# Kernel tuning notes

Measured on AMD Instinct MI355X. Metric: run time of the kernel, lower is better.

Reference implementation:

```python
import jax, jax.numpy as jnp
import numpy as np

B, D, U, M, K = 8192, 512, 512, 16, 64


def setup_inputs() -> dict:
    key = jax.random.key(0)
    ks = jax.random.split(key, 5)
    return {
        "x": jax.random.normal(ks[0], (B, D), dtype=jnp.float32),
        "key_kernel": jax.random.normal(ks[1], (D, K), dtype=jnp.float32) * (1.0 / np.sqrt(D)),
        "key_bias": jnp.zeros((K,), dtype=jnp.float32),
        "keys_map": jax.random.normal(ks[2], (M, K), dtype=jnp.float32),
        "kernels": jax.random.normal(ks[3], (M, D, U), dtype=jnp.float32) * (1.0 / np.sqrt(D)),
        "biases": jnp.zeros((M, U), dtype=jnp.float32),
    }


def reference(x, key_kernel, key_bias, keys_map, kernels, biases):
    # key projection: [B, K]
    keyv = x @ key_kernel + key_bias
    # inverse-distance similarity to mode keys: [B, M]
    dist = jnp.sqrt(jnp.sum((keyv[:, None, :] - keys_map[None, :, :]) ** 2, axis=-1))
    sim = 1.0 / (dist + 1.0)
    modes = kernels.shape[0]
    # kernel = mean_m(sim_m * kernels_m); out = x @ kernel.
    # Distributive identity: out = (1/M) * sum_m sim_m * (x @ kernels_m)
    out = jnp.einsum("bm,bd,mdu->bu", sim, x, kernels) / modes
    # bias = mean_m(sim_m * biases_m): [B, U]
    out = out + (sim @ biases) / modes
    return out
```

## Files before the change

### kernel.cpp

```cpp
#include <hip/hip_runtime.h>
#include <hip/hip_bf16.h>
#include <stdint.h>

#define B_SZ 8192
#define D_SZ 512
#define U_SZ 512
#define M_SZ 16
#define K_SZ 64

#define BROWS 64
#define BU 128
#define BK 64

typedef short bf16x8 __attribute__((ext_vector_type(8)));
typedef float f32x4 __attribute__((ext_vector_type(4)));

__device__ __forceinline__ unsigned short f2bf(float f) {
  union { float f; unsigned u; } v; v.f = f;
  unsigned r = v.u + 0x7fffu + ((v.u >> 16) & 1u);
  return (unsigned short)(r >> 16);
}

__device__ __forceinline__ void async16(const void* gptr, void* ldsptr) {
  __builtin_amdgcn_global_load_lds(
      (const __attribute__((address_space(1))) unsigned int*)gptr,
      (__attribute__((address_space(3))) unsigned int*)ldsptr,
      16, 0, 0);
}

__global__ __launch_bounds__(256) void cvt_kT(const float* __restrict__ kin,
                                              unsigned short* __restrict__ kT) {
  __shared__ float tf[32][65];
  int m = blockIdx.z, d0 = blockIdx.y * 32, u0 = blockIdx.x * 64;
  int t = threadIdx.x;
  {
    int dr = t >> 4, uc = t & 15;
    const float* src = kin + ((size_t)(m * D_SZ + d0 + dr)) * U_SZ + u0 + uc * 4;
    float4 a = *(const float4*)src;
    float4 b = *(const float4*)(src + 16 * U_SZ);
    tf[dr][uc * 4 + 0] = a.x; tf[dr][uc * 4 + 1] = a.y;
    tf[dr][uc * 4 + 2] = a.z; tf[dr][uc * 4 + 3] = a.w;
    tf[dr + 16][uc * 4 + 0] = b.x; tf[dr + 16][uc * 4 + 1] = b.y;
    tf[dr + 16][uc * 4 + 2] = b.z; tf[dr + 16][uc * 4 + 3] = b.w;
  }
  __syncthreads();
  {
    int ur = t >> 2, dc = t & 3;
    unsigned short* dst = kT + ((size_t)(m * U_SZ + u0 + ur)) * D_SZ + d0 + dc * 8;
    ushort4 lo, hi;
    lo.x = f2bf(tf[dc * 8 + 0][ur]); lo.y = f2bf(tf[dc * 8 + 1][ur]);
    lo.z = f2bf(tf[dc * 8 + 2][ur]); lo.w = f2bf(tf[dc * 8 + 3][ur]);
    hi.x = f2bf(tf[dc * 8 + 4][ur]); hi.y = f2bf(tf[dc * 8 + 5][ur]);
    hi.z = f2bf(tf[dc * 8 + 6][ur]); hi.w = f2bf(tf[dc * 8 + 7][ur]);
    *(ushort4*)dst = lo;
    *(ushort4*)(dst + 4) = hi;
  }
}

__global__ __launch_bounds__(256) void sim_kernel(
    const float* __restrict__ x, const float* __restrict__ key_kernel,
    const float* __restrict__ key_bias, const float* __restrict__ keys_map,
    float* __restrict__ sim, unsigned short* __restrict__ xb) {
  __shared__ float xs[16 * 512];
  __shared__ float ks[64 * 64];
  __shared__ float kv[16 * 64];
  int t = threadIdx.x;
  int b0 = blockIdx.x * 16;
  const float4* xg = (const float4*)(x + (size_t)b0 * D_SZ);
  float4* xs4 = (float4*)xs;
  ushort4* xb4 = (ushort4*)(xb + (size_t)b0 * D_SZ);
#pragma unroll
  for (int q = 0; q < 8; ++q) {
    float4 v = xg[q * 256 + t];
    xs4[q * 256 + t] = v;
    ushort4 o;
    o.x = f2bf(v.x); o.y = f2bf(v.y); o.z = f2bf(v.z); o.w = f2bf(v.w);
    xb4[q * 256 + t] = o;
  }
  int row = t >> 4, tk = t & 15;
  float4 acc = *(const float4*)(key_bias + tk * 4);
  float4* ks4 = (float4*)ks;
  const float4* wk4 = (const float4*)key_kernel;
  for (int c = 0; c < 8; ++c) {
    __syncthreads();
#pragma unroll
    for (int q = 0; q < 4; ++q) ks4[q * 256 + t] = wk4[c * 1024 + q * 256 + t];
    __syncthreads();
    const float* xrow = xs + row * 512 + c * 64;
#pragma unroll 8
    for (int dd = 0; dd < 64; ++dd) {
      float4 kk = ks4[dd * 16 + tk];
      float xv = xrow[dd];
      acc.x += xv * kk.x; acc.y += xv * kk.y;
      acc.z += xv * kk.z; acc.w += xv * kk.w;
    }
  }
  *(float4*)(kv + row * 64 + tk * 4) = acc;
  __syncthreads();
  int mm = t & 15;
  const float* kvr = kv + row * 64;
  const float* km = keys_map + mm * 64;
  float d2 = 0.f;
#pragma unroll 8
  for (int k = 0; k < 64; ++k) {
    float df = kvr[k] - km[k];
    d2 += df * df;
  }
  sim[(size_t)(b0 + row) * M_SZ + mm] = 1.0f / (sqrtf(d2) + 1.0f);
}

__global__ __launch_bounds__(256, 2) void poly_gemm(
    const unsigned short* __restrict__ xb,
    const unsigned short* __restrict__ kT,
    const float* __restrict__ sim,
    const float* __restrict__ biases,
    float* __restrict__ out) {
  __shared__ unsigned short sA[BROWS * D_SZ];
  __shared__ unsigned short sB[BU * BK];

  int t = threadIdx.x;
  int w = t >> 6, l = t & 63;
  int bid = blockIdx.x;
  int ut = (bid & 7) >> 1;
  int bt = ((bid >> 3) << 1) | (bid & 1);
  int b0 = bt * BROWS;
  int u0 = ut * BU;

  const unsigned short* xsrc = xb + (size_t)b0 * D_SZ;
#pragma unroll
  for (int c = 0; c < 16; ++c) {
    int ch = w * 16 + c;
    async16(xsrc + (size_t)ch * D_SZ + (size_t)(l ^ (ch & 7)) * 8,
            (char*)sA + ch * 1024);
  }

  int wi = w >> 1, wj = w & 1;
  int rbase = wi * 32, cbase = wj * 64;
  int lane16 = l & 15, quad = l >> 4;
  int sw = lane16 & 7;

  f32x4 facc[2][4];
#pragma unroll
  for (int i = 0; i < 2; ++i)
#pragma unroll
    for (int j = 0; j < 4; ++j) facc[i][j] = (f32x4){0.f, 0.f, 0.f, 0.f};

  for (int m = 0; m < M_SZ; ++m) {
    f32x4 pacc[2][4];
#pragma unroll
    for (int i = 0; i < 2; ++i)
#pragma unroll
      for (int j = 0; j < 4; ++j) pacc[i][j] = (f32x4){0.f, 0.f, 0.f, 0.f};

    const unsigned short* bsrc = kT + ((size_t)m * U_SZ + u0) * D_SZ;
    for (int kt = 0; kt < D_SZ / BK; ++kt) {
      __syncthreads();
#pragma unroll
      for (int c = 0; c < 4; ++c) {
        int ch = w * 4 + c;
        int urow = ch * 8 + (l >> 3);
        int kk8 = ((l & 7) ^ (l >> 3)) * 8;
        async16(bsrc + (size_t)urow * D_SZ + kt * BK + kk8, (char*)sB + ch * 1024);
      }
      __syncthreads();
#pragma unroll
      for (int h = 0; h < 2; ++h) {
        bf16x8 af[2], bfr[4];
        int ckA = kt * 8 + h * 4 + quad;
        int pA = ckA ^ sw;
#pragma unroll
        for (int i = 0; i < 2; ++i)
          af[i] = *(const bf16x8*)(sA + (size_t)(rbase + i * 16 + lane16) * D_SZ + pA * 8);
        int ckB = h * 4 + quad;
        int pB = ckB ^ sw;
#pragma unroll
        for (int j = 0; j < 4; ++j)
          bfr[j] = *(const bf16x8*)(sB + (size_t)(cbase + j * 16 + lane16) * BK + pB * 8);
#pragma unroll
        for (int i = 0; i < 2; ++i)
#pragma unroll
          for (int j = 0; j < 4; ++j)
            pacc[i][j] = __builtin_amdgcn_mfma_f32_16x16x32_bf16(
                af[i], bfr[j], pacc[i][j], 0, 0, 0);
      }
    }
    float bv[4];
#pragma unroll
    for (int j = 0; j < 4; ++j)
      bv[j] = biases[(size_t)m * U_SZ + u0 + cbase + j * 16 + lane16];
#pragma unroll
    for (int i = 0; i < 2; ++i)
#pragma unroll
      for (int r = 0; r < 4; ++r) {
        int row = b0 + rbase + i * 16 + quad * 4 + r;
        float s = sim[(size_t)row * M_SZ + m];
#pragma unroll
        for (int j = 0; j < 4; ++j)
          facc[i][j][r] += s * (pacc[i][j][r] + bv[j]);
      }
  }

  float* orow = out + (size_t)b0 * U_SZ + u0;
#pragma unroll
  for (int i = 0; i < 2; ++i)
#pragma unroll
    for (int r = 0; r < 4; ++r) {
      int row = rbase + i * 16 + quad * 4 + r;
#pragma unroll
      for (int j = 0; j < 4; ++j)
        orow[(size_t)row * U_SZ + cbase + j * 16 + lane16] =
            facc[i][j][r] * 0.0625f;
    }
}

extern "C" void kernel_launch(void* const* d_in, const int* in_sizes, int n_in,
                              void* d_out, int out_size, void* d_ws, size_t ws_size,
                              hipStream_t stream) {
  const float* x = (const float*)d_in[0];
  const float* key_kernel = (const float*)d_in[1];
  const float* key_bias = (const float*)d_in[2];
  const float* keys_map = (const float*)d_in[3];
  const float* kernels = (const float*)d_in[4];
  const float* biases = (const float*)d_in[5];
  float* out = (float*)d_out;

  unsigned short* xb = (unsigned short*)d_ws;
  unsigned short* kT = xb + (size_t)B_SZ * D_SZ;
  float* sim = (float*)((char*)d_ws + 2 * (size_t)B_SZ * D_SZ +
                        2 * (size_t)M_SZ * U_SZ * D_SZ);

  cvt_kT<<<dim3(U_SZ / 64, D_SZ / 32, M_SZ), 256, 0, stream>>>(kernels, kT);
  sim_kernel<<<dim3(B_SZ / 16), 256, 0, stream>>>(x, key_kernel, key_bias,
                                                  keys_map, sim, xb);
  poly_gemm<<<dim3(512), 256, 0, stream>>>(xb, kT, sim, biases, out);
}
```

Measured before the change: 197.3 us.

## Merge prep kernels and restructure poly GEMM with k-outer, m-inner double-buffered loop

Merges the kernel transpose/convert and the similarity kernel into a single prep launch, which also writes the bias term into the output. The GEMM is restructured to tiles of 128 rows by 64 columns. It loops over the K dimension outermost and the 16 modes inner, so A fragments are reused across modes and B tiles are double-buffered with async loads one iteration ahead. Similarities are stored transposed for vector loads, and the GEMM accumulates into the output instead of storing it. The risks are an extra global read-modify-write of the output and more sim-scaling ALU work per MFMA pair, since partial products are scaled per k-chunk.

```diff
diff --git a/kernel.cpp b/kernel.cpp
--- a/kernel.cpp
+++ b/kernel.cpp
@@ -8,10 +8,6 @@
 #define M_SZ 16
 #define K_SZ 64
 
-#define BROWS 64
-#define BU 128
-#define BK 64
-
 typedef short bf16x8 __attribute__((ext_vector_type(8)));
 typedef float f32x4 __attribute__((ext_vector_type(4)));
 
@@ -28,188 +24,237 @@
       16, 0, 0);
 }
 
-__global__ __launch_bounds__(256) void cvt_kT(const float* __restrict__ kin,
-                                              unsigned short* __restrict__ kT) {
-  __shared__ float tf[32][65];
-  int m = blockIdx.z, d0 = blockIdx.y * 32, u0 = blockIdx.x * 64;
-  int t = threadIdx.x;
-  {
-    int dr = t >> 4, uc = t & 15;
-    const float* src = kin + ((size_t)(m * D_SZ + d0 + dr)) * U_SZ + u0 + uc * 4;
-    float4 a = *(const float4*)src;
-    float4 b = *(const float4*)(src + 16 * U_SZ);
-    tf[dr][uc * 4 + 0] = a.x; tf[dr][uc * 4 + 1] = a.y;
-    tf[dr][uc * 4 + 2] = a.z; tf[dr][uc * 4 + 3] = a.w;
-    tf[dr + 16][uc * 4 + 0] = b.x; tf[dr + 16][uc * 4 + 1] = b.y;
-    tf[dr + 16][uc * 4 + 2] = b.z; tf[dr + 16][uc * 4 + 3] = b.w;
-  }
-  __syncthreads();
-  {
-    int ur = t >> 2, dc = t & 3;
-    unsigned short* dst = kT + ((size_t)(m * U_SZ + u0 + ur)) * D_SZ + d0 + dc * 8;
-    ushort4 lo, hi;
-    lo.x = f2bf(tf[dc * 8 + 0][ur]); lo.y = f2bf(tf[dc * 8 + 1][ur]);
-    lo.z = f2bf(tf[dc * 8 + 2][ur]); lo.w = f2bf(tf[dc * 8 + 3][ur]);
-    hi.x = f2bf(tf[dc * 8 + 4][ur]); hi.y = f2bf(tf[dc * 8 + 5][ur]);
-    hi.z = f2bf(tf[dc * 8 + 6][ur]); hi.w = f2bf(tf[dc * 8 + 7][ur]);
-    *(ushort4*)dst = lo;
-    *(ushort4*)(dst + 4) = hi;
-  }
-}
-
-__global__ __launch_bounds__(256) void sim_kernel(
+__global__ __launch_bounds__(256) void prep(
     const float* __restrict__ x, const float* __restrict__ key_kernel,
     const float* __restrict__ key_bias, const float* __restrict__ keys_map,
-    float* __restrict__ sim, unsigned short* __restrict__ xb) {
-  __shared__ float xs[16 * 512];
-  __shared__ float ks[64 * 64];
-  __shared__ float kv[16 * 64];
+    const float* __restrict__ kernels, const float* __restrict__ biases,
+    unsigned short* __restrict__ xb, unsigned short* __restrict__ kT,
+    float* __restrict__ simT, float* __restrict__ out) {
+  __shared__ float smem[13568];
+  int bid = blockIdx.x;
   int t = threadIdx.x;
-  int b0 = blockIdx.x * 16;
-  const float4* xg = (const float4*)(x + (size_t)b0 * D_SZ);
-  float4* xs4 = (float4*)xs;
-  ushort4* xb4 = (ushort4*)(xb + (size_t)b0 * D_SZ);
-#pragma unroll
-  for (int q = 0; q < 8; ++q) {
-    float4 v = xg[q * 256 + t];
-    xs4[q * 256 + t] = v;
-    ushort4 o;
-    o.x = f2bf(v.x); o.y = f2bf(v.y); o.z = f2bf(v.z); o.w = f2bf(v.w);
-    xb4[q * 256 + t] = o;
-  }
-  int row = t >> 4, tk = t & 15;
-  float4 acc = *(const float4*)(key_bias + tk * 4);
-  float4* ks4 = (float4*)ks;
-  const float4* wk4 = (const float4*)key_kernel;
-  for (int c = 0; c < 8; ++c) {
+
+  if (bid < 2048) {
+    float(*tf)[65] = (float(*)[65])smem;
+    int m = bid >> 7;
+    int rem = bid & 127;
+    int d0 = ((rem >> 3) & 15) * 32, u0 = (rem & 7) * 64;
+    {
+      int dr = t >> 4, uc = t & 15;
+      const float* src = kernels + ((size_t)m * D_SZ + d0 + dr) * U_SZ + u0 + uc * 4;
+      float4 a = *(const float4*)src;
+      float4 b = *(const float4*)(src + (size_t)16 * U_SZ);
+      tf[dr][uc * 4 + 0] = a.x; tf[dr][uc * 4 + 1] = a.y;
+      tf[dr][uc * 4 + 2] = a.z; tf[dr][uc * 4 + 3] = a.w;
+      tf[dr + 16][uc * 4 + 0] = b.x; tf[dr + 16][uc * 4 + 1] = b.y;
+      tf[dr + 16][uc * 4 + 2] = b.z; tf[dr + 16][uc * 4 + 3] = b.w;
+    }
     __syncthreads();
-#pragma unroll
-    for (int q = 0; q < 4; ++q) ks4[q * 256 + t] = wk4[c * 1024 + q * 256 + t];
-    __syncthreads();
-    const float* xrow = xs + row * 512 + c * 64;
+    {
+      int ur = t >> 2, dc = t & 3;
+      unsigned short* dst = kT + ((size_t)m * U_SZ + u0 + ur) * D_SZ + d0 + dc * 8;
+      ushort4 lo, hi;
+      lo.x = f2bf(tf[dc * 8 + 0][ur]); lo.y = f2bf(tf[dc * 8 + 1][ur]);
+      lo.z = f2bf(tf[dc * 8 + 2][ur]); lo.w = f2bf(tf[dc * 8 + 3][ur]);
+      hi.x = f2bf(tf[dc * 8 + 4][ur]); hi.y = f2bf(tf[dc * 8 + 5][ur]);
+      hi.z = f2bf(tf[dc * 8 + 6][ur]); hi.w = f2bf(tf[dc * 8 + 7][ur]);
+      *(ushort4*)dst = lo;
+      *(ushort4*)(dst + 4) = hi;
+    }
+    return;
+  }
+
+  float* xs = smem;
+  float* wk = smem + 8192;
+  float* kv = smem + 12288;
+  float* sims = smem + 13312;
+  int b0 = (bid - 2048) * 16;
+
+  {
+    const float4* xg = (const float4*)(x + (size_t)b0 * D_SZ);
+    float4* xs4 = (float4*)xs;
+    ushort4* xb4 = (ushort4*)(xb + (size_t)b0 * D_SZ);
+#pragma unroll
+    for (int p = 0; p < 8; ++p) {
+      int idx = p * 256 + t;
+      float4 v = xg[idx];
+      xs4[idx] = v;
+      ushort4 o;
+      o.x = f2bf(v.x); o.y = f2bf(v.y); o.z = f2bf(v.z); o.w = f2bf(v.w);
+      xb4[idx] = o;
+    }
+  }
+
+  int row = t >> 4, kq = t & 15;
+  float4 acc = *(const float4*)(key_bias + kq * 4);
+  {
+    float4* wk4 = (float4*)wk;
+    const float4* wg = (const float4*)key_kernel;
+    for (int c = 0; c < 8; ++c) {
+      __syncthreads();
+#pragma unroll
+      for (int q = 0; q < 4; ++q) wk4[q * 256 + t] = wg[c * 1024 + q * 256 + t];
+      __syncthreads();
+      const float* xrow = xs + row * 512 + c * 64;
 #pragma unroll 8
-    for (int dd = 0; dd < 64; ++dd) {
-      float4 kk = ks4[dd * 16 + tk];
-      float xv = xrow[dd];
-      acc.x += xv * kk.x; acc.y += xv * kk.y;
-      acc.z += xv * kk.z; acc.w += xv * kk.w;
-    }
-  }
-  *(float4*)(kv + row * 64 + tk * 4) = acc;
+      for (int dd = 0; dd < 64; ++dd) {
+        float4 kk = wk4[dd * 16 + kq];
+        float xv = xrow[dd];
+        acc.x += xv * kk.x; acc.y += xv * kk.y;
+        acc.z += xv * kk.z; acc.w += xv * kk.w;
+      }
+    }
+  }
+  *(float4*)(kv + row * 64 + kq * 4) = acc;
   __syncthreads();
-  int mm = t & 15;
-  const float* kvr = kv + row * 64;
-  const float* km = keys_map + mm * 64;
-  float d2 = 0.f;
+
+  {
+    int mm = t & 15;
+    const float* kvr = kv + row * 64;
+    const float* km = keys_map + mm * 64;
+    float d2 = 0.f;
 #pragma unroll 8
-  for (int k = 0; k < 64; ++k) {
-    float df = kvr[k] - km[k];
-    d2 += df * df;
-  }
-  sim[(size_t)(b0 + row) * M_SZ + mm] = 1.0f / (sqrtf(d2) + 1.0f);
+    for (int k = 0; k < 64; ++k) {
+      float df = kvr[k] - km[k];
+      d2 += df * df;
+    }
+    float s = 1.0f / (sqrtf(d2) + 1.0f);
+    simT[(size_t)mm * B_SZ + b0 + row] = s;
+    sims[row * 16 + mm] = s;
+  }
+  __syncthreads();
+
+  {
+    const float4* bg = (const float4*)biases;
+    float4* og = (float4*)(out + (size_t)b0 * U_SZ);
+#pragma unroll
+    for (int p = 0; p < 8; ++p) {
+      int idx = p * 256 + t;
+      int r2 = idx >> 7, uc = idx & 127;
+      float4 a4 = {0.f, 0.f, 0.f, 0.f};
+#pragma unroll
+      for (int mm = 0; mm < 16; ++mm) {
+        float s = sims[r2 * 16 + mm];
+        float4 b4 = bg[mm * 128 + uc];
+        a4.x += s * b4.x; a4.y += s * b4.y; a4.z += s * b4.z; a4.w += s * b4.w;
+      }
+      a4.x *= 0.0625f; a4.y *= 0.0625f; a4.z *= 0.0625f; a4.w *= 0.0625f;
+      og[idx] = a4;
+    }
+  }
 }
 
 __global__ __launch_bounds__(256, 2) void poly_gemm(
     const unsigned short* __restrict__ xb,
     const unsigned short* __restrict__ kT,
-    const float* __restrict__ sim,
-    const float* __restrict__ biases,
+    const float* __restrict__ simT,
     float* __restrict__ out) {
-  __shared__ unsigned short sA[BROWS * D_SZ];
-  __shared__ unsigned short sB[BU * BK];
-
-  int t = threadIdx.x;
-  int w = t >> 6, l = t & 63;
+  __shared__ unsigned short sA[128 * 64];
+  __shared__ unsigned short sB[2 * 64 * 64];
+
+  int t = threadIdx.x, w = t >> 6, l = t & 63;
   int bid = blockIdx.x;
-  int ut = (bid & 7) >> 1;
-  int bt = ((bid >> 3) << 1) | (bid & 1);
-  int b0 = bt * BROWS;
-  int u0 = ut * BU;
-
-  const unsigned short* xsrc = xb + (size_t)b0 * D_SZ;
-#pragma unroll
-  for (int c = 0; c < 16; ++c) {
-    int ch = w * 16 + c;
-    async16(xsrc + (size_t)ch * D_SZ + (size_t)(l ^ (ch & 7)) * 8,
-            (char*)sA + ch * 1024);
-  }
-
-  int wi = w >> 1, wj = w & 1;
-  int rbase = wi * 32, cbase = wj * 64;
-  int lane16 = l & 15, quad = l >> 4;
-  int sw = lane16 & 7;
+  int ut = bid & 7, bt = bid >> 3;
+  int b0 = bt * 128, u0 = ut * 64;
+
+  int rbase = w * 32;
+  int lane16 = l & 15, quad = l >> 4, sw = lane16 & 7;
+  int srow = l >> 3;
+  int skk = ((l & 7) ^ srow) * 8;
+
+  const unsigned short* asrc = xb + (size_t)b0 * D_SZ;
+
+#pragma unroll
+  for (int c = 0; c < 4; ++c) {
+    int ch = w * 4 + c;
+    int row = ch * 8 + srow;
+    async16(asrc + (size_t)row * D_SZ + skk, (char*)sA + ch * 1024);
+  }
+#pragma unroll
+  for (int c = 0; c < 2; ++c) {
+    int ch = w * 2 + c;
+    int row = ch * 8 + srow;
+    async16(kT + ((size_t)u0 + row) * D_SZ + skk, (char*)sB + ch * 1024);
+  }
 
   f32x4 facc[2][4];
 #pragma unroll
   for (int i = 0; i < 2; ++i)
 #pragma unroll
     for (int j = 0; j < 4; ++j) facc[i][j] = (f32x4){0.f, 0.f, 0.f, 0.f};
-
-  for (int m = 0; m < M_SZ; ++m) {
-    f32x4 pacc[2][4];
-#pragma unroll
-    for (int i = 0; i < 2; ++i)
-#pragma unroll
-      for (int j = 0; j < 4; ++j) pacc[i][j] = (f32x4){0.f, 0.f, 0.f, 0.f};
-
-    const unsigned short* bsrc = kT + ((size_t)m * U_SZ + u0) * D_SZ;
-    for (int kt = 0; kt < D_SZ / BK; ++kt) {
-      __syncthreads();
+  bf16x8 af[2][2];
+
+#pragma unroll 1
+  for (int iter = 0; iter < 128; ++iter) {
+    int kt = iter >> 4, m = iter & 15;
+    __syncthreads();
+
+    int nit = iter + 1;
+    if (nit < 128) {
+      int nm = nit & 15, nkt = nit >> 4;
+      const unsigned short* bsrc = kT + ((size_t)nm * U_SZ + u0) * D_SZ + nkt * 64;
+      char* dst = (char*)sB + (nit & 1) * 8192;
+#pragma unroll
+      for (int c = 0; c < 2; ++c) {
+        int ch = w * 2 + c;
+        int row = ch * 8 + srow;
+        async16(bsrc + (size_t)row * D_SZ + skk, dst + ch * 1024);
+      }
+    }
+    if (m == 15 && kt < 7) {
 #pragma unroll
       for (int c = 0; c < 4; ++c) {
         int ch = w * 4 + c;
-        int urow = ch * 8 + (l >> 3);
-        int kk8 = ((l & 7) ^ (l >> 3)) * 8;
-        async16(bsrc + (size_t)urow * D_SZ + kt * BK + kk8, (char*)sB + ch * 1024);
-      }
-      __syncthreads();
-#pragma unroll
-      for (int h = 0; h < 2; ++h) {
-        bf16x8 af[2], bfr[4];
-        int ckA = kt * 8 + h * 4 + quad;
-        int pA = ckA ^ sw;
-#pragma unroll
-        for (int i = 0; i < 2; ++i)
-          af[i] = *(const bf16x8*)(sA + (size_t)(rbase + i * 16 + lane16) * D_SZ + pA * 8);
-        int ckB = h * 4 + quad;
-        int pB = ckB ^ sw;
-#pragma unroll
-        for (int j = 0; j < 4; ++j)
-          bfr[j] = *(const bf16x8*)(sB + (size_t)(cbase + j * 16 + lane16) * BK + pB * 8);
-#pragma unroll
-        for (int i = 0; i < 2; ++i)
-#pragma unroll
-          for (int j = 0; j < 4; ++j)
-            pacc[i][j] = __builtin_amdgcn_mfma_f32_16x16x32_bf16(
-                af[i], bfr[j], pacc[i][j], 0, 0, 0);
-      }
-    }
-    float bv[4];
+        int row = ch * 8 + srow;
+        async16(asrc + (size_t)row * D_SZ + (kt + 1) * 64 + skk,
+                (char*)sA + ch * 1024);
+      }
+    }
+    if (m == 0) {
+#pragma unroll
+      for (int i = 0; i < 2; ++i)
+#pragma unroll
+        for (int h = 0; h < 2; ++h)
+          af[i][h] = *(const bf16x8*)(sA + (size_t)(rbase + i * 16 + lane16) * 64 +
+                                      (((h * 4 + quad) ^ sw) * 8));
+    }
+
+    const unsigned short* sBc = sB + (iter & 1) * 4096;
+    bf16x8 bfr[4][2];
 #pragma unroll
     for (int j = 0; j < 4; ++j)
-      bv[j] = biases[(size_t)m * U_SZ + u0 + cbase + j * 16 + lane16];
+#pragma unroll
+      for (int h = 0; h < 2; ++h)
+        bfr[j][h] = *(const bf16x8*)(sBc + (size_t)(j * 16 + lane16) * 64 +
+                                     (((h * 4 + quad) ^ sw) * 8));
+
+    f32x4 sv[2];
 #pragma unroll
     for (int i = 0; i < 2; ++i)
-#pragma unroll
-      for (int r = 0; r < 4; ++r) {
-        int row = b0 + rbase + i * 16 + quad * 4 + r;
-        float s = sim[(size_t)row * M_SZ + m];
-#pragma unroll
-        for (int j = 0; j < 4; ++j)
-          facc[i][j][r] += s * (pacc[i][j][r] + bv[j]);
-      }
-  }
-
-  float* orow = out + (size_t)b0 * U_SZ + u0;
+      sv[i] = *(const f32x4*)(simT + (size_t)m * B_SZ + b0 + rbase + i * 16 +
+                              quad * 4);
+
+#pragma unroll
+    for (int i = 0; i < 2; ++i)
+#pragma unroll
+      for (int j = 0; j < 4; ++j) {
+        f32x4 p = __builtin_amdgcn_mfma_f32_16x16x32_bf16(
+            af[i][0], bfr[j][0], (f32x4){0.f, 0.f, 0.f, 0.f}, 0, 0, 0);
+        p = __builtin_amdgcn_mfma_f32_16x16x32_bf16(af[i][1], bfr[j][1], p, 0, 0, 0);
+#pragma unroll
+        for (int r = 0; r < 4; ++r) facc[i][j][r] += sv[i][r] * p[r];
+      }
+  }
+
 #pragma unroll
   for (int i = 0; i < 2; ++i)
 #pragma unroll
     for (int r = 0; r < 4; ++r) {
-      int row = rbase + i * 16 + quad * 4 + r;
+      int row = b0 + rbase + i * 16 + quad * 4 + r;
+      float* orow = out + (size_t)row * U_SZ + u0;
 #pragma unroll
       for (int j = 0; j < 4; ++j)
-        orow[(size_t)row * U_SZ + cbase + j * 16 + lane16] =
-            facc[i][j][r] * 0.0625f;
+        orow[j * 16 + lane16] += facc[i][j][r] * 0.0625f;
     }
 }
 
@@ -224,13 +269,12 @@
   const float* biases = (const float*)d_in[5];
   float* out = (float*)d_out;
 
-  unsigned short* xb = (unsigned short*)d_ws;
-  unsigned short* kT = xb + (size_t)B_SZ * D_SZ;
-  float* sim = (float*)((char*)d_ws + 2 * (size_t)B_SZ * D_SZ +
-                        2 * (size_t)M_SZ * U_SZ * D_SZ);
-
-  cvt_kT<<<dim3(U_SZ / 64, D_SZ / 32, M_SZ), 256, 0, stream>>>(kernels, kT);
-  sim_kernel<<<dim3(B_SZ / 16), 256, 0, stream>>>(x, key_kernel, key_bias,
-                                                  keys_map, sim, xb);
-  poly_gemm<<<dim3(512), 256, 0, stream>>>(xb, kT, sim, biases, out);
-}
+  char* p = (char*)d_ws;
+  unsigned short* xb = (unsigned short*)p;  p += (size_t)B_SZ * D_SZ * 2;
+  unsigned short* kT = (unsigned short*)p;  p += (size_t)M_SZ * U_SZ * D_SZ * 2;
+  float* simT = (float*)p;
+
+  prep<<<dim3(2560), 256, 0, stream>>>(x, key_kernel, key_bias, keys_map,
+                                       kernels, biases, xb, kT, simT, out);
+  poly_gemm<<<dim3(512), 256, 0, stream>>>(xb, kT, simT, out);
+}
```

Result: slower. 234.2 us (+18.7%).
